# Performance work log

Measured on AMD Instinct MI355X. Metric: run time of the kernel, lower is better.

Reference implementation:

```python
import jax, jax.numpy as jnp
import numpy as np

EPS = 1e-5   # BatchNorm3d eps
SLOPE = 0.01 # LeakyReLU default negative_slope

def conv3(x, w, pad):
    return jax.lax.conv_general_dilated(
        x, w, (1, 1, 1), [(pad, pad)] * 3,
        dimension_numbers=('NCDHW', 'OIDHW', 'NCDHW'))

def bn(x):
    # BatchNorm3d in training mode with affine init (weight=1, bias=0):
    # normalize by per-channel batch statistics (biased variance).
    m = x.mean(axis=(0, 2, 3, 4), keepdims=True)
    v = x.var(axis=(0, 2, 3, 4), keepdims=True)
    return (x - m) / jnp.sqrt(v + EPS)

def lrelu(x):
    return jnp.where(x >= 0, x, SLOPE * x)

def block(x, w1, w2):
    # ConvBlock: conv3x3x3 -> BN -> LeakyReLU, twice
    x = lrelu(bn(conv3(x, w1, 1)))
    return lrelu(bn(conv3(x, w2, 1)))

def maxpool2(x):
    # MaxPool3dMPS(kernel=2, stride=2, pad=0) == standard 2x2x2 maxpool
    B, C, D, H, W = x.shape
    return x.reshape(B, C, D // 2, 2, H // 2, 2, W // 2, 2).max(axis=(3, 5, 7))

def upconv_fft(x, w):
    # ConvTranspose3dMPS: nearest-neighbor upsample by stride=2 via repeat,
    # then per-(out,in)-channel CIRCULAR convolution implemented with FFTs
    # (weight zero-padded to the upsampled spatial shape). Vectorized here
    # over all channel pairs with a frequency-domain einsum; rfft is used
    # since all signals are real (identical math, half the memory).
    s = 2
    B, C, D, H, W = x.shape
    up = jnp.broadcast_to(x[:, :, :, None, :, None, :, None],
                          (B, C, D, s, H, s, W, s)).reshape(B, C, D * s, H * s, W * s)
    sp = up.shape[2:]
    X = jnp.fft.rfftn(up, axes=(2, 3, 4))                 # [B, Cin, D', H', Wf]
    Wf = jnp.fft.rfftn(w, s=sp, axes=(2, 3, 4))           # [Cout, Cin, D', H', Wf]
    Y = jnp.einsum('bidhw,oidhw->bodhw', X, Wf)
    return jnp.fft.irfftn(Y, s=sp, axes=(2, 3, 4))

def unet_fwd(x, wf1, wf2, wd1a, wd1b, wd2a, wd2b, wd3a, wd3b,
             wt1, wu1a, wu1b, wt2, wu2a, wu2b, wt3, wu3a, wu3b,
             w_final, b_final):
    x1 = block(x, wf1, wf2)                       # [B,16,64,64,64]
    x2 = block(maxpool2(x1), wd1a, wd1b)          # [B,32,32,32,32]
    x3 = block(maxpool2(x2), wd2a, wd2b)          # [B,64,16,16,16]
    x4 = block(maxpool2(x3), wd3a, wd3b)          # [B,128,8,8,8]

    def up(a, skip, wt, wa, wb):
        u = lrelu(bn(upconv_fft(a, wt)))
        return block(jnp.concatenate([skip, u], axis=1), wa, wb)

    a = up(x4, x3, wt1, wu1a, wu1b)               # [B,64,16,16,16]
    a = up(a, x2, wt2, wu2a, wu2b)                # [B,32,32,32,32]
    a = up(a, x1, wt3, wu3a, wu3b)                # [B,16,64,64,64]
    return conv3(a, w_final, 0) + b_final.reshape(1, -1, 1, 1, 1)

def setup_inputs() -> dict:
    key = jax.random.key(0)
    ks = jax.random.split(key, 32)
    def W(k, shape):
        fan = int(np.prod(shape[1:]))
        return jax.random.normal(k, shape, jnp.float32) * np.float32((2.0 / fan) ** 0.5)
    inp = {}
    inp['x'] = jax.random.normal(ks[0], (1, 1, 64, 64, 64), jnp.float32)
    shapes = {
        'wf1': (16, 1, 3, 3, 3),  'wf2': (16, 16, 3, 3, 3),
        'wd1a': (32, 16, 3, 3, 3), 'wd1b': (32, 32, 3, 3, 3),
        'wd2a': (64, 32, 3, 3, 3), 'wd2b': (64, 64, 3, 3, 3),
        'wd3a': (128, 64, 3, 3, 3), 'wd3b': (128, 128, 3, 3, 3),
        'wt1': (64, 128, 2, 2, 2), 'wu1a': (64, 128, 3, 3, 3), 'wu1b': (64, 64, 3, 3, 3),
        'wt2': (32, 64, 2, 2, 2),  'wu2a': (32, 64, 3, 3, 3),  'wu2b': (32, 32, 3, 3, 3),
        'wt3': (16, 32, 2, 2, 2),  'wu3a': (16, 32, 3, 3, 3),  'wu3b': (16, 16, 3, 3, 3),
        'w_final': (1, 16, 1, 1, 1),
    }
    for i, (name, sh) in enumerate(shapes.items()):
        inp[name] = W(ks[i + 1], sh)
    inp['b_final'] = jnp.zeros((1,), jnp.float32)
    return inp

def reference(x, wf1, wf2, wd1a, wd1b, wd2a, wd2b, wd3a, wd3b,
              wt1, wu1a, wu1b, wt2, wu2a, wu2b, wt3, wu3a, wu3b,
              w_final, b_final):
    return unet_fwd(x, wf1, wf2, wd1a, wd1b, wd2a, wd2b, wd3a, wd3b,
                    wt1, wu1a, wu1b, wt2, wu2a, wu2b, wt3, wu3a, wu3b,
                    w_final, b_final)
```

## Files before the change

### kernel.cpp

```cpp
#include <hip/hip_runtime.h>

#define EPS   1e-5f
#define SLOPE 0.01f

template <int CIN, int CC, int BT>
__global__ __launch_bounds__(BT) void conv3_q9(const float* __restrict__ in,
                                               const float* __restrict__ wt,
                                               float* __restrict__ part,
                                               int D, int H, int W) {
    const int V    = D * H * W;
    const int Cout = gridDim.x * 8;
    const int z    = blockIdx.z;
    const int cib  = z * CC;
    __shared__ float wlds[27 * CC * 8];
    const int co0 = blockIdx.x * 8;
    for (int i = threadIdx.x; i < 27 * CC * 8; i += BT) {
        const int co = i & 7;
        const int t2 = i >> 3;
        const int tap = t2 % 3;
        const int t3  = t2 / 3;
        const int ci  = t3 % CC;
        const int pl  = t3 / CC;
        wlds[i] = wt[((size_t)(co0 + co) * CIN + cib + ci) * 27 + pl * 3 + tap];
    }
    __syncthreads();

    const float* inz = in + (size_t)cib * V;
    const int v0 = (blockIdx.y * BT + threadIdx.x) * 4;
    const int w0 = v0 % W;
    const int h0 = (v0 / W) % H;
    const int d0 = v0 / (W * H);

    const bool mL = (w0 != 0);
    const bool mR = (w0 + 4 != W);
    const int  wl = w0 - (mL ? 1 : 0);
    const int  wr = w0 + (mR ? 4 : 3);

    float acc[32];
#pragma unroll
    for (int i = 0; i < 32; ++i) acc[i] = 0.f;

#pragma unroll 1
    for (int kd = 0; kd < 3; ++kd) {
#pragma unroll 1
        for (int kh = 0; kh < 3; ++kh) {
            const int zd = d0 + kd - 1, zh = h0 + kh - 1;
            const bool okp = ((unsigned)zd < (unsigned)D) & ((unsigned)zh < (unsigned)H);
            const int row = okp ? (zd * H + zh) * W : 0;
            const int pl  = kd * 3 + kh;
            const float* wpl = &wlds[pl * CC * 24];
#pragma unroll 2
            for (int ci = 0; ci < CC; ++ci) {
                const float* p = inz + (size_t)ci * V + row;
                float4 m = *(const float4*)(p + w0);
                float lv = p[wl];
                float rv = p[wr];
                if (!okp) { m.x = 0.f; m.y = 0.f; m.z = 0.f; m.w = 0.f; }
                if (!(okp && mL)) lv = 0.f;
                if (!(okp && mR)) rv = 0.f;
                const float* wb = wpl + ci * 24;
                const float4 w0a = *(const float4*)(wb);
                const float4 w0b = *(const float4*)(wb + 4);
                const float4 w1a = *(const float4*)(wb + 8);
                const float4 w1b = *(const float4*)(wb + 12);
                const float4 w2a = *(const float4*)(wb + 16);
                const float4 w2b = *(const float4*)(wb + 20);
#define FMA4(A0, A1, A2, AP)                                                    \
                {                                                               \
                    float* a = (AP);                                            \
                    a[0] = fmaf(lv,  (A0), fmaf(m.x, (A1), fmaf(m.y, (A2), a[0])));\
                    a[1] = fmaf(m.x, (A0), fmaf(m.y, (A1), fmaf(m.z, (A2), a[1])));\
                    a[2] = fmaf(m.y, (A0), fmaf(m.z, (A1), fmaf(m.w, (A2), a[2])));\
                    a[3] = fmaf(m.z, (A0), fmaf(m.w, (A1), fmaf(rv,  (A2), a[3])));\
                }
                FMA4(w0a.x, w0b.x, w1a.x, acc + 0);
#undef FMA4
                (void)0;
#define FMA4C(A0, A1, A2, AP)                                                   \
                {                                                               \
                    float* a = (AP);                                            \
                    a[0] = fmaf(lv,  (A0), fmaf(m.x, (A1), fmaf(m.y, (A2), a[0])));\
                    a[1] = fmaf(m.x, (A0), fmaf(m.y, (A1), fmaf(m.z, (A2), a[1])));\
                    a[2] = fmaf(m.y, (A0), fmaf(m.z, (A1), fmaf(m.w, (A2), a[2])));\
                    a[3] = fmaf(m.z, (A0), fmaf(m.w, (A1), fmaf(rv,  (A2), a[3])));\
                }
                FMA4C(w0a.y, w1a.y, w2a.y, acc + 4);
                FMA4C(w0a.z, w1a.z, w2a.z, acc + 8);
                FMA4C(w0a.w, w1a.w, w2a.w, acc + 12);
                FMA4C(w0b.x, w1b.x, w2b.x, acc + 16);
                FMA4C(w0b.y, w1b.y, w2b.y, acc + 20);
                FMA4C(w0b.z, w1b.z, w2b.z, acc + 24);
                FMA4C(w0b.w, w1b.w, w2b.w, acc + 28);
#undef FMA4C
            }
        }
    }
#pragma unroll
    for (int co = 0; co < 8; ++co)
        *(float4*)&part[((size_t)z * Cout + co0 + co) * V + v0] = *(const float4*)&acc[co * 4];
}

template <int CIN, int CC, int BT>
__global__ __launch_bounds__(BT) void conv3_qA(const float* __restrict__ in,
                                               const float* __restrict__ wt,
                                               float* __restrict__ part,
                                               int D, int H, int W) {
    const int V    = D * H * W;
    const int Cout = gridDim.x * 8;
    const int z    = blockIdx.z;
    const int cib  = z * CC;
    __shared__ float wlds[27 * CC * 8];
    const int co0 = blockIdx.x * 8;
    for (int i = threadIdx.x; i < 27 * CC * 8; i += BT) {
        const int co  = i & 7;
        const int t2  = i >> 3;
        const int tap = t2 % 3;
        const int t3  = t2 / 3;
        const int ci  = t3 % CC;
        const int pl  = t3 / CC;
        wlds[i] = wt[((size_t)(co0 + co) * CIN + cib + ci) * 27 + pl * 3 + tap];
    }
    __syncthreads();

    const float* inz = in + (size_t)cib * V;
    const int v0 = (blockIdx.y * BT + threadIdx.x) * 4;
    const int w0 = v0 % W;
    const int h0 = (v0 / W) % H;
    const int d0 = v0 / (W * H);

    const bool mL = (w0 != 0);
    const bool mR = (w0 + 4 != W);
    const int  wl = w0 - (mL ? 1 : 0);
    const int  wr = w0 + (mR ? 4 : 3);

    float acc[32];
#pragma unroll
    for (int i = 0; i < 32; ++i) acc[i] = 0.f;

#pragma unroll 1
    for (int kd = 0; kd < 3; ++kd) {
#pragma unroll 1
        for (int kh = 0; kh < 3; ++kh) {
            const int zd = d0 + kd - 1, zh = h0 + kh - 1;
            const bool okp = ((unsigned)zd < (unsigned)D) & ((unsigned)zh < (unsigned)H);
            const int row = okp ? (zd * H + zh) * W : 0;
            const float* wpl = &wlds[(kd * 3 + kh) * CC * 24];
#pragma unroll 2
            for (int ci = 0; ci < CC; ++ci) {
                const float* p = inz + (size_t)ci * V + row;
                float4 m = *(const float4*)(p + w0);
                float lv = p[wl];
                float rv = p[wr];
                if (!okp) { m.x = 0.f; m.y = 0.f; m.z = 0.f; m.w = 0.f; }
                if (!(okp && mL)) lv = 0.f;
                if (!(okp && mR)) rv = 0.f;
                const float* wb = wpl + ci * 24;
                const float4 t0a = *(const float4*)(wb);
                const float4 t0b = *(const float4*)(wb + 4);
                const float4 t1a = *(const float4*)(wb + 8);
                const float4 t1b = *(const float4*)(wb + 12);
                const float4 t2a = *(const float4*)(wb + 16);
                const float4 t2b = *(const float4*)(wb + 20);
#define FMA4C(A0, A1, A2, AP)                                                       \
                {                                                                   \
                    float* a = (AP);                                                \
                    a[0] = fmaf(lv,  (A0), fmaf(m.x, (A1), fmaf(m.y, (A2), a[0]))); \
                    a[1] = fmaf(m.x, (A0), fmaf(m.y, (A1), fmaf(m.z, (A2), a[1]))); \
                    a[2] = fmaf(m.y, (A0), fmaf(m.z, (A1), fmaf(m.w, (A2), a[2]))); \
                    a[3] = fmaf(m.z, (A0), fmaf(m.w, (A1), fmaf(rv,  (A2), a[3]))); \
                }
                FMA4C(t0a.x, t1a.x, t2a.x, acc + 0);
                FMA4C(t0a.y, t1a.y, t2a.y, acc + 4);
                FMA4C(t0a.z, t1a.z, t2a.z, acc + 8);
                FMA4C(t0a.w, t1a.w, t2a.w, acc + 12);
                FMA4C(t0b.x, t1b.x, t2b.x, acc + 16);
                FMA4C(t0b.y, t1b.y, t2b.y, acc + 20);
                FMA4C(t0b.z, t1b.z, t2b.z, acc + 24);
                FMA4C(t0b.w, t1b.w, t2b.w, acc + 28);
#undef FMA4C
            }
        }
    }
#pragma unroll
    for (int co = 0; co < 8; ++co)
        *(float4*)&part[((size_t)z * Cout + co0 + co) * V + v0] = *(const float4*)&acc[co * 4];
}

template <int CIN, int CC, int VOXB>
__global__ __launch_bounds__(256) void upconv_v8(const float* __restrict__ in,
                                                 const float* __restrict__ wt,
                                                 float* __restrict__ part,
                                                 int Di, int Hi, int Wi) {
    const int Do = 2 * Di, Ho = 2 * Hi, Wo = 2 * Wi;
    const int Vo = Do * Ho * Wo;
    const int Vi = Di * Hi * Wi;
    const int Cout = gridDim.x * 8;
    const int z    = blockIdx.z;
    const int cib  = z * CC;
    __shared__ float wlds[8 * CC * 8];
    const int co0 = blockIdx.x * 8;
    for (int i = threadIdx.x; i < 8 * CC * 8; i += 256) {
        const int co  = i & 7;
        const int t2  = i >> 3;
        const int ci  = t2 % CC;
        const int tap = t2 / CC;
        wlds[i] = wt[((size_t)(co0 + co) * CIN + cib + ci) * 8 + tap];
    }
    __syncthreads();

    const float* inz = in + (size_t)cib * Vi;
    const int vbase = blockIdx.y * (256 * VOXB) + threadIdx.x;
    int od[VOXB], oh[VOXB], ow[VOXB];
#pragma unroll
    for (int j = 0; j < VOXB; ++j) {
        const int v = vbase + j * 256;
        ow[j] = v % Wo;
        oh[j] = (v / Wo) % Ho;
        od[j] = v / (Wo * Ho);
    }
    float acc[8 * VOXB];
#pragma unroll
    for (int i = 0; i < 8 * VOXB; ++i) acc[i] = 0.f;

#pragma unroll 1
    for (int kd = 0; kd < 2; ++kd)
#pragma unroll 1
    for (int kh = 0; kh < 2; ++kh)
#pragma unroll
    for (int kw = 0; kw < 2; ++kw) {
        const int tap = (kd * 2 + kh) * 2 + kw;
        int sp[VOXB];
#pragma unroll
        for (int j = 0; j < VOXB; ++j) {
            const int id = ((od[j] - kd + Do) & (Do - 1)) >> 1;
            const int ih = ((oh[j] - kh + Ho) & (Ho - 1)) >> 1;
            const int iw = ((ow[j] - kw + Wo) & (Wo - 1)) >> 1;
            sp[j] = (id * Hi + ih) * Wi + iw;
        }
        const float* wrow = &wlds[tap * CC * 8];
#pragma unroll 2
        for (int ci = 0; ci < CC; ++ci) {
            float xv[VOXB];
#pragma unroll
            for (int j = 0; j < VOXB; ++j)
                xv[j] = inz[(size_t)ci * Vi + sp[j]];
            const float4 wa = *(const float4*)(wrow + ci * 8);
            const float4 wb = *(const float4*)(wrow + ci * 8 + 4);
#define UF(WC, CO)                                                              \
            {                                                                   \
                _Pragma("unroll")                                               \
                for (int j = 0; j < VOXB; ++j)                                  \
                    acc[(CO) * VOXB + j] = fmaf(xv[j], (WC), acc[(CO) * VOXB + j]); \
            }
            UF(wa.x, 0) UF(wa.y, 1) UF(wa.z, 2) UF(wa.w, 3)
            UF(wb.x, 4) UF(wb.y, 5) UF(wb.z, 6) UF(wb.w, 7)
#undef UF
        }
    }
#pragma unroll
    for (int co = 0; co < 8; ++co)
#pragma unroll
        for (int j = 0; j < VOXB; ++j)
            part[((size_t)z * Cout + co0 + co) * Vo + vbase + j * 256] = acc[co * VOXB + j];
}

__global__ __launch_bounds__(256) void bn_stats_part_v2(const float* __restrict__ part,
                                                        float* __restrict__ pstat,
                                                        int C, int V, int S, int chunk) {
    const int c = blockIdx.x, seg = blockIdx.y;
    const size_t base = (size_t)c * V + (size_t)seg * chunk;
    float s1 = 0.f, s2 = 0.f;
    for (int i = threadIdx.x * 4; i < chunk; i += 1024) {
        float4 t = make_float4(0.f, 0.f, 0.f, 0.f);
        for (int s = 0; s < S; ++s) {
            const float4 v = *(const float4*)(part + (size_t)s * C * V + base + i);
            t.x += v.x; t.y += v.y; t.z += v.z; t.w += v.w;
        }
        s1 += t.x + t.y + t.z + t.w;
        s2 = fmaf(t.x, t.x, fmaf(t.y, t.y, fmaf(t.z, t.z, fmaf(t.w, t.w, s2))));
    }
#pragma unroll
    for (int off = 32; off > 0; off >>= 1) {
        s1 += __shfl_down(s1, off, 64);
        s2 += __shfl_down(s2, off, 64);
    }
    __shared__ float sh[8];
    const int wid  = threadIdx.x >> 6;
    const int lane = threadIdx.x & 63;
    if (lane == 0) { sh[wid] = s1; sh[4 + wid] = s2; }
    __syncthreads();
    if (threadIdx.x == 0) {
        pstat[(c * gridDim.y + seg) * 2]     = sh[0] + sh[1] + sh[2] + sh[3];
        pstat[(c * gridDim.y + seg) * 2 + 1] = sh[4] + sh[5] + sh[6] + sh[7];
    }
}

__global__ __launch_bounds__(64) void bn_stats_final(const float* __restrict__ pstat,
                                                     float* __restrict__ stats,
                                                     int S, int V) {
    const int c = blockIdx.x;
    float s1 = 0.f, s2 = 0.f;
    if ((int)threadIdx.x < S) {
        s1 = pstat[(c * S + threadIdx.x) * 2];
        s2 = pstat[(c * S + threadIdx.x) * 2 + 1];
    }
#pragma unroll
    for (int off = 32; off > 0; off >>= 1) {
        s1 += __shfl_down(s1, off, 64);
        s2 += __shfl_down(s2, off, 64);
    }
    if (threadIdx.x == 0) {
        const float inv  = 1.f / (float)V;
        const float mean = s1 * inv;
        const float var  = s2 * inv - mean * mean;
        stats[2 * c]     = mean;
        stats[2 * c + 1] = rsqrtf(var + EPS);
    }
}

__global__ __launch_bounds__(256) void bn_apply_v3(const float* __restrict__ part,
                                                   float* __restrict__ dst,
                                                   const float* __restrict__ stats,
                                                   int C, int V4, int S, int total4) {
    const int idx = blockIdx.x * blockDim.x + threadIdx.x;
    if (idx >= total4) return;
    const int c = idx / V4;
    const int v = idx - c * V4;
    const float4* p4 = (const float4*)part;
    float4 t = make_float4(0.f, 0.f, 0.f, 0.f);
    for (int s = 0; s < S; ++s) {
        const float4 x = p4[(size_t)(s * C + c) * V4 + v];
        t.x += x.x; t.y += x.y; t.z += x.z; t.w += x.w;
    }
    const float mean = stats[2 * c];
    const float rstd = stats[2 * c + 1];
    float u;
    u = (t.x - mean) * rstd; t.x = u >= 0.f ? u : SLOPE * u;
    u = (t.y - mean) * rstd; t.y = u >= 0.f ? u : SLOPE * u;
    u = (t.z - mean) * rstd; t.z = u >= 0.f ? u : SLOPE * u;
    u = (t.w - mean) * rstd; t.w = u >= 0.f ? u : SLOPE * u;
    ((float4*)dst)[idx] = t;
}

__global__ __launch_bounds__(256) void maxpool_kernel(const float* __restrict__ in,
                                                      float* __restrict__ out,
                                                      int D, int H, int W, int total) {
    const int Do = D >> 1, Ho = H >> 1, Wo = W >> 1;
    const int Vo = Do * Ho * Wo;
    const int idx = blockIdx.x * blockDim.x + threadIdx.x;
    if (idx >= total) return;
    const int c  = idx / Vo;
    const int v  = idx - c * Vo;
    const int ow = v % Wo;
    const int oh = (v / Wo) % Ho;
    const int od = v / (Wo * Ho);
    const size_t HW = (size_t)H * W;
    const float* p = in + (size_t)c * D * HW + (size_t)(2 * od) * HW + (size_t)(2 * oh) * W + 2 * ow;
    float m = p[0];
    m = fmaxf(m, p[1]);
    m = fmaxf(m, p[W]);
    m = fmaxf(m, p[W + 1]);
    m = fmaxf(m, p[HW]);
    m = fmaxf(m, p[HW + 1]);
    m = fmaxf(m, p[HW + W]);
    m = fmaxf(m, p[HW + W + 1]);
    out[idx] = m;
}

__global__ __launch_bounds__(256) void final_v2(const float* __restrict__ in,
                                                const float* __restrict__ w,
                                                const float* __restrict__ b,
                                                float* __restrict__ out, int C, int V4) {
    const int idx = blockIdx.x * blockDim.x + threadIdx.x;
    if (idx >= V4) return;
    const float bb = b[0];
    float4 acc = make_float4(bb, bb, bb, bb);
    for (int c = 0; c < C; ++c) {
        const float4 v = ((const float4*)in)[(size_t)c * V4 + idx];
        const float wc = w[c];
        acc.x = fmaf(v.x, wc, acc.x);
        acc.y = fmaf(v.y, wc, acc.y);
        acc.z = fmaf(v.z, wc, acc.z);
        acc.w = fmaf(v.w, wc, acc.w);
    }
    ((float4*)out)[idx] = acc;
}


extern "C" void kernel_launch(void* const* d_in, const int* in_sizes, int n_in,
                              void* d_out, int out_size, void* d_ws, size_t ws_size,
                              hipStream_t stream) {
    const float* x      = (const float*)d_in[0];
    const float* wf1    = (const float*)d_in[1];
    const float* wf2    = (const float*)d_in[2];
    const float* wd1a   = (const float*)d_in[3];
    const float* wd1b   = (const float*)d_in[4];
    const float* wd2a   = (const float*)d_in[5];
    const float* wd2b   = (const float*)d_in[6];
    const float* wd3a   = (const float*)d_in[7];
    const float* wd3b   = (const float*)d_in[8];
    const float* wt1    = (const float*)d_in[9];
    const float* wu1a   = (const float*)d_in[10];
    const float* wu1b   = (const float*)d_in[11];
    const float* wt2    = (const float*)d_in[12];
    const float* wu2a   = (const float*)d_in[13];
    const float* wu2b   = (const float*)d_in[14];
    const float* wt3    = (const float*)d_in[15];
    const float* wu3a   = (const float*)d_in[16];
    const float* wu3b   = (const float*)d_in[17];
    const float* w_fin  = (const float*)d_in[18];
    const float* b_fin  = (const float*)d_in[19];
    float* out = (float*)d_out;

    const int V0 = 64 * 64 * 64;
    const int V1 = 32 * 32 * 32;
    const int V2 = 16 * 16 * 16;
    const int V3 = 8 * 8 * 8;

    float* ws    = (float*)d_ws;
    float* cat3  = ws;
    float* cat2  = cat3 + (size_t)32 * V0;
    float* cat1  = cat2 + (size_t)64 * V1;
    float* x4    = cat1 + (size_t)128 * V2;
    float* tA    = x4   + (size_t)128 * V3;
    float* tB    = tA   + (size_t)16 * V0;
    float* part  = tB   + (size_t)16 * V0;
    float* stats = part + (size_t)16 * V0;
    float* pstat = stats + 256;

    auto blocks = [](int n) { return (n + 255) / 256; };

    auto bn_lrelu = [&](const float* p, float* dstp, int C, int V, int S) {
        const int NSEG = (V >= V0) ? 16 : (V == V1) ? 8 : (V == V2) ? 2 : 1;
        hipLaunchKernelGGL(bn_stats_part_v2, dim3(C, NSEG), dim3(256), 0, stream,
                           p, pstat, C, V, S, V / NSEG);
        hipLaunchKernelGGL(bn_stats_final, dim3(C), dim3(64), 0, stream, pstat, stats, NSEG, V);
        const int total4 = C * V / 4;
        hipLaunchKernelGGL(bn_apply_v3, dim3(blocks(total4)), dim3(256), 0, stream,
                           p, dstp, stats, C, V / 4, S, total4);
    };
    auto maxpool = [&](const float* in, float* o, int C, int D, int H, int W) {
        const int total = C * (D / 2) * (H / 2) * (W / 2);
        hipLaunchKernelGGL(maxpool_kernel, dim3(blocks(total)), dim3(256), 0, stream,
                           in, o, D, H, W, total);
    };

#define CONVQ(CIN, CC, BT, in_, wt_, prt_, dst_, Cout, D_, H_, W_)                          \
    {                                                                                       \
        const int V_ = (D_) * (H_) * (W_);                                                  \
        const int S  = (CIN) / (CC);                                                        \
        dim3 g((Cout) / 8, V_ / (4 * (BT)), S);                                             \
        hipLaunchKernelGGL((conv3_qA<CIN, CC, BT>), g, dim3(BT), 0, stream,                 \
                           in_, wt_, prt_, D_, H_, W_);                                     \
        bn_lrelu(prt_, dst_, Cout, V_, S);                                                  \
    }
#define UPCONV(CIN, CC, VOXB, in_, wt_, prt_, dst_, Cout, Di_, Hi_, Wi_)                    \
    {                                                                                       \
        const int Vo_ = 8 * (Di_) * (Hi_) * (Wi_);                                          \
        const int S  = (CIN) / (CC);                                                        \
        dim3 g((Cout) / 8, Vo_ / (256 * (VOXB)), S);                                        \
        hipLaunchKernelGGL((upconv_v8<CIN, CC, VOXB>), g, dim3(256), 0, stream,             \
                           in_, wt_, prt_, Di_, Hi_, Wi_);                                  \
        bn_lrelu(prt_, dst_, Cout, Vo_, S);                                                 \
    }

    CONVQ(1,   1,  256, x,   wf1,  tA,   tA,          16, 64, 64, 64);
    CONVQ(16,  8,  256, tA,  wf2,  tB,   cat3,        16, 64, 64, 64);
    maxpool(cat3, tA, 16, 64, 64, 64);
    CONVQ(16,  8,  64,  tA,  wd1a, part, tB,          32, 32, 32, 32);
    CONVQ(32,  8,  64,  tB,  wd1b, part, cat2,        32, 32, 32, 32);
    maxpool(cat2, tA, 32, 32, 32, 32);
    CONVQ(32,  8,  64,  tA,  wd2a, part, tB,          64, 16, 16, 16);
    CONVQ(64,  8,  64,  tB,  wd2b, part, cat1,        64, 16, 16, 16);
    maxpool(cat1, tA, 64, 16, 16, 16);
    CONVQ(64,  4,  64,  tA,  wd3a, part, tB,         128, 8, 8, 8);
    CONVQ(128, 8,  64,  tB,  wd3b, part, x4,         128, 8, 8, 8);

    UPCONV(128, 16, 1, x4, wt1, part, cat1 + (size_t)64 * V2, 64, 8, 8, 8);
    CONVQ(128, 8,  64, cat1, wu1a, part, tA,          64, 16, 16, 16);
    CONVQ(64,  8,  64, tA,   wu1b, part, tB,          64, 16, 16, 16);

    UPCONV(64, 16, 1, tB, wt2, part, cat2 + (size_t)32 * V1, 32, 16, 16, 16);
    CONVQ(64, 16, 64, cat2, wu2a, part, tA,           32, 32, 32, 32);
    CONVQ(32, 8,  64, tA,   wu2b, part, tB,           32, 32, 32, 32);

    {
        float* up3dst = cat3 + (size_t)16 * V0;
        UPCONV(32, 32, 4, tB, wt3, up3dst, up3dst, 16, 32, 32, 32);
    }
    CONVQ(32, 16, 256, cat3, wu3a, tB,   tA,          16, 64, 64, 64);
    CONVQ(16, 8,  256, tA,   wu3b, cat3, tB,          16, 64, 64, 64);

    hipLaunchKernelGGL(final_v2, dim3(blocks(V0 / 4)), dim3(256), 0, stream,
                       tB, w_fin, b_fin, out, 16, V0 / 4);

#undef CONVQ
#undef UPCONV
}
```

Baseline: 1.054 ms.

## Fuse BN statistics into full-resolution conv and upconv kernels, drop split-K partials

For the 64^3 layers, the convolution now runs over all input channels in one block instead of splitting input channels across grid z, so no partial sums are written and re-reduced. Per-block sums and sums of squares are computed in the conv epilogue, and a new bn_apply_f kernel finishes the statistics and applies normalization plus LeakyReLU in a single pass. The last upconv gets a matching fused-stats kernel. This removes the separate stats passes over large activations, at the cost of less grid parallelism, larger LDS weight tiles (up to 27*32*8 floats), and variance computed as E[x^2]-mean^2 in fp32, which is less numerically stable.

```diff
diff --git a/kernel.cpp b/kernel.cpp
--- a/kernel.cpp
+++ b/kernel.cpp
@@ -3,34 +3,32 @@
 #define EPS   1e-5f
 #define SLOPE 0.01f
 
-template <int CIN, int CC, int BT>
-__global__ __launch_bounds__(BT) void conv3_q9(const float* __restrict__ in,
-                                               const float* __restrict__ wt,
-                                               float* __restrict__ part,
-                                               int D, int H, int W) {
-    const int V    = D * H * W;
-    const int Cout = gridDim.x * 8;
-    const int z    = blockIdx.z;
-    const int cib  = z * CC;
-    __shared__ float wlds[27 * CC * 8];
+template <int CIN, int BT>
+__global__ __launch_bounds__(BT) void conv3_big(const float* __restrict__ in,
+                                                const float* __restrict__ wt,
+                                                float* __restrict__ out,
+                                                float* __restrict__ bstat,
+                                                int D, int H, int W) {
+    const int V   = D * H * W;
+    const int NB  = gridDim.y;
     const int co0 = blockIdx.x * 8;
-    for (int i = threadIdx.x; i < 27 * CC * 8; i += BT) {
-        const int co = i & 7;
-        const int t2 = i >> 3;
-        const int tap = t2 % 3;
-        const int t3  = t2 / 3;
-        const int ci  = t3 % CC;
-        const int pl  = t3 / CC;
-        wlds[i] = wt[((size_t)(co0 + co) * CIN + cib + ci) * 27 + pl * 3 + tap];
-    }
-    __syncthreads();
-
-    const float* inz = in + (size_t)cib * V;
+    __shared__ float wlds[27 * CIN * 8];
+    __shared__ float sred[(BT / 64) * 16];
+    for (int i = threadIdx.x; i < 27 * CIN * 8; i += BT) {
+        const int co  = i & 7;
+        const int r   = i >> 3;
+        const int tap = r % 3;
+        const int r2  = r / 3;
+        const int pl  = r2 % 9;
+        const int ci  = r2 / 9;
+        wlds[i] = wt[((size_t)(co0 + co) * CIN + ci) * 27 + pl * 3 + tap];
+    }
+    __syncthreads();
+
     const int v0 = (blockIdx.y * BT + threadIdx.x) * 4;
     const int w0 = v0 % W;
     const int h0 = (v0 / W) % H;
     const int d0 = v0 / (W * H);
-
     const bool mL = (w0 != 0);
     const bool mR = (w0 + 4 != W);
     const int  wl = w0 - (mL ? 1 : 0);
@@ -41,63 +39,239 @@
     for (int i = 0; i < 32; ++i) acc[i] = 0.f;
 
 #pragma unroll 1
-    for (int kd = 0; kd < 3; ++kd) {
-#pragma unroll 1
-        for (int kh = 0; kh < 3; ++kh) {
-            const int zd = d0 + kd - 1, zh = h0 + kh - 1;
-            const bool okp = ((unsigned)zd < (unsigned)D) & ((unsigned)zh < (unsigned)H);
-            const int row = okp ? (zd * H + zh) * W : 0;
-            const int pl  = kd * 3 + kh;
-            const float* wpl = &wlds[pl * CC * 24];
-#pragma unroll 2
-            for (int ci = 0; ci < CC; ++ci) {
-                const float* p = inz + (size_t)ci * V + row;
+    for (int ci = 0; ci < CIN; ++ci) {
+        const float* pc = in + (size_t)ci * V;
+#pragma unroll 1
+        for (int kd = 0; kd < 3; ++kd) {
+#pragma unroll 1
+            for (int kh = 0; kh < 3; ++kh) {
+                const int zd = d0 + kd - 1, zh = h0 + kh - 1;
+                const bool okp = ((unsigned)zd < (unsigned)D) & ((unsigned)zh < (unsigned)H);
+                const int row = okp ? (zd * H + zh) * W : 0;
+                const float* p = pc + row;
                 float4 m = *(const float4*)(p + w0);
                 float lv = p[wl];
                 float rv = p[wr];
                 if (!okp) { m.x = 0.f; m.y = 0.f; m.z = 0.f; m.w = 0.f; }
                 if (!(okp && mL)) lv = 0.f;
                 if (!(okp && mR)) rv = 0.f;
-                const float* wb = wpl + ci * 24;
-                const float4 w0a = *(const float4*)(wb);
-                const float4 w0b = *(const float4*)(wb + 4);
-                const float4 w1a = *(const float4*)(wb + 8);
-                const float4 w1b = *(const float4*)(wb + 12);
-                const float4 w2a = *(const float4*)(wb + 16);
-                const float4 w2b = *(const float4*)(wb + 20);
-#define FMA4(A0, A1, A2, AP)                                                    \
-                {                                                               \
-                    float* a = (AP);                                            \
-                    a[0] = fmaf(lv,  (A0), fmaf(m.x, (A1), fmaf(m.y, (A2), a[0])));\
-                    a[1] = fmaf(m.x, (A0), fmaf(m.y, (A1), fmaf(m.z, (A2), a[1])));\
-                    a[2] = fmaf(m.y, (A0), fmaf(m.z, (A1), fmaf(m.w, (A2), a[2])));\
-                    a[3] = fmaf(m.z, (A0), fmaf(m.w, (A1), fmaf(rv,  (A2), a[3])));\
+                const float* wb = &wlds[((ci * 9 + kd * 3 + kh) * 3) * 8];
+                const float4 t0a = *(const float4*)(wb);
+                const float4 t0b = *(const float4*)(wb + 4);
+                const float4 t1a = *(const float4*)(wb + 8);
+                const float4 t1b = *(const float4*)(wb + 12);
+                const float4 t2a = *(const float4*)(wb + 16);
+                const float4 t2b = *(const float4*)(wb + 20);
+#define FMA4C(A0, A1, A2, AP)                                                       \
+                {                                                                   \
+                    float* a = (AP);                                                \
+                    a[0] = fmaf(lv,  (A0), fmaf(m.x, (A1), fmaf(m.y, (A2), a[0]))); \
+                    a[1] = fmaf(m.x, (A0), fmaf(m.y, (A1), fmaf(m.z, (A2), a[1]))); \
+                    a[2] = fmaf(m.y, (A0), fmaf(m.z, (A1), fmaf(m.w, (A2), a[2]))); \
+                    a[3] = fmaf(m.z, (A0), fmaf(m.w, (A1), fmaf(rv,  (A2), a[3]))); \
                 }
-                FMA4(w0a.x, w0b.x, w1a.x, acc + 0);
-#undef FMA4
-                (void)0;
-#define FMA4C(A0, A1, A2, AP)                                                   \
-                {                                                               \
-                    float* a = (AP);                                            \
-                    a[0] = fmaf(lv,  (A0), fmaf(m.x, (A1), fmaf(m.y, (A2), a[0])));\
-                    a[1] = fmaf(m.x, (A0), fmaf(m.y, (A1), fmaf(m.z, (A2), a[1])));\
-                    a[2] = fmaf(m.y, (A0), fmaf(m.z, (A1), fmaf(m.w, (A2), a[2])));\
-                    a[3] = fmaf(m.z, (A0), fmaf(m.w, (A1), fmaf(rv,  (A2), a[3])));\
-                }
-                FMA4C(w0a.y, w1a.y, w2a.y, acc + 4);
-                FMA4C(w0a.z, w1a.z, w2a.z, acc + 8);
-                FMA4C(w0a.w, w1a.w, w2a.w, acc + 12);
-                FMA4C(w0b.x, w1b.x, w2b.x, acc + 16);
-                FMA4C(w0b.y, w1b.y, w2b.y, acc + 20);
-                FMA4C(w0b.z, w1b.z, w2b.z, acc + 24);
-                FMA4C(w0b.w, w1b.w, w2b.w, acc + 28);
+                FMA4C(t0a.x, t1a.x, t2a.x, acc + 0);
+                FMA4C(t0a.y, t1a.y, t2a.y, acc + 4);
+                FMA4C(t0a.z, t1a.z, t2a.z, acc + 8);
+                FMA4C(t0a.w, t1a.w, t2a.w, acc + 12);
+                FMA4C(t0b.x, t1b.x, t2b.x, acc + 16);
+                FMA4C(t0b.y, t1b.y, t2b.y, acc + 20);
+                FMA4C(t0b.z, t1b.z, t2b.z, acc + 24);
+                FMA4C(t0b.w, t1b.w, t2b.w, acc + 28);
 #undef FMA4C
             }
         }
     }
 #pragma unroll
     for (int co = 0; co < 8; ++co)
-        *(float4*)&part[((size_t)z * Cout + co0 + co) * V + v0] = *(const float4*)&acc[co * 4];
+        *(float4*)&out[(size_t)(co0 + co) * V + v0] = *(const float4*)&acc[co * 4];
+
+    float s1[8], s2[8];
+#pragma unroll
+    for (int co = 0; co < 8; ++co) {
+        const float* a = &acc[co * 4];
+        s1[co] = a[0] + a[1] + a[2] + a[3];
+        s2[co] = fmaf(a[0], a[0], fmaf(a[1], a[1], fmaf(a[2], a[2], a[3] * a[3])));
+    }
+#pragma unroll
+    for (int off = 32; off > 0; off >>= 1)
+#pragma unroll
+        for (int co = 0; co < 8; ++co) {
+            s1[co] += __shfl_down(s1[co], off, 64);
+            s2[co] += __shfl_down(s2[co], off, 64);
+        }
+    const int lane = threadIdx.x & 63;
+    const int wv   = threadIdx.x >> 6;
+    if (lane == 0)
+#pragma unroll
+        for (int co = 0; co < 8; ++co) {
+            sred[(wv * 8 + co) * 2]     = s1[co];
+            sred[(wv * 8 + co) * 2 + 1] = s2[co];
+        }
+    __syncthreads();
+    if ((int)threadIdx.x < 8) {
+        float S1 = 0.f, S2 = 0.f;
+#pragma unroll
+        for (int w = 0; w < BT / 64; ++w) {
+            S1 += sred[(w * 8 + threadIdx.x) * 2];
+            S2 += sred[(w * 8 + threadIdx.x) * 2 + 1];
+        }
+        bstat[((size_t)(co0 + threadIdx.x) * NB + blockIdx.y) * 2]     = S1;
+        bstat[((size_t)(co0 + threadIdx.x) * NB + blockIdx.y) * 2 + 1] = S2;
+    }
+}
+
+template <int CIN>
+__global__ __launch_bounds__(256) void upconv_big(const float* __restrict__ in,
+                                                  const float* __restrict__ wt,
+                                                  float* __restrict__ out,
+                                                  float* __restrict__ bstat,
+                                                  int Di, int Hi, int Wi) {
+    const int Do = 2 * Di, Ho = 2 * Hi, Wo = 2 * Wi;
+    const int Vo = Do * Ho * Wo;
+    const int Vi = Di * Hi * Wi;
+    const int NB = gridDim.y;
+    const int co0 = blockIdx.x * 8;
+    __shared__ float wlds[8 * CIN * 8];
+    __shared__ float sred[4 * 16];
+    for (int i = threadIdx.x; i < 8 * CIN * 8; i += 256) {
+        const int co  = i & 7;
+        const int t2  = i >> 3;
+        const int ci  = t2 % CIN;
+        const int tap = t2 / CIN;
+        wlds[i] = wt[((size_t)(co0 + co) * CIN + ci) * 8 + tap];
+    }
+    __syncthreads();
+
+    const int vbase = blockIdx.y * 1024 + threadIdx.x;
+    int od[4], oh[4], ow[4];
+#pragma unroll
+    for (int j = 0; j < 4; ++j) {
+        const int v = vbase + j * 256;
+        ow[j] = v % Wo;
+        oh[j] = (v / Wo) % Ho;
+        od[j] = v / (Wo * Ho);
+    }
+    float acc[32];
+#pragma unroll
+    for (int i = 0; i < 32; ++i) acc[i] = 0.f;
+
+#pragma unroll 1
+    for (int kd = 0; kd < 2; ++kd)
+#pragma unroll 1
+    for (int kh = 0; kh < 2; ++kh)
+#pragma unroll
+    for (int kw = 0; kw < 2; ++kw) {
+        const int tap = (kd * 2 + kh) * 2 + kw;
+        int sp[4];
+#pragma unroll
+        for (int j = 0; j < 4; ++j) {
+            const int id = ((od[j] - kd + Do) & (Do - 1)) >> 1;
+            const int ih = ((oh[j] - kh + Ho) & (Ho - 1)) >> 1;
+            const int iw = ((ow[j] - kw + Wo) & (Wo - 1)) >> 1;
+            sp[j] = (id * Hi + ih) * Wi + iw;
+        }
+        const float* wrow = &wlds[tap * CIN * 8];
+#pragma unroll 2
+        for (int ci = 0; ci < CIN; ++ci) {
+            float xv[4];
+#pragma unroll
+            for (int j = 0; j < 4; ++j)
+                xv[j] = in[(size_t)ci * Vi + sp[j]];
+            const float4 wa = *(const float4*)(wrow + ci * 8);
+            const float4 wb = *(const float4*)(wrow + ci * 8 + 4);
+#define UF(WC, CO)                                                              \
+            {                                                                   \
+                _Pragma("unroll")                                               \
+                for (int j = 0; j < 4; ++j)                                     \
+                    acc[(CO) * 4 + j] = fmaf(xv[j], (WC), acc[(CO) * 4 + j]);   \
+            }
+            UF(wa.x, 0) UF(wa.y, 1) UF(wa.z, 2) UF(wa.w, 3)
+            UF(wb.x, 4) UF(wb.y, 5) UF(wb.z, 6) UF(wb.w, 7)
+#undef UF
+        }
+    }
+#pragma unroll
+    for (int co = 0; co < 8; ++co)
+#pragma unroll
+        for (int j = 0; j < 4; ++j)
+            out[(size_t)(co0 + co) * Vo + vbase + j * 256] = acc[co * 4 + j];
+
+    float s1[8], s2[8];
+#pragma unroll
+    for (int co = 0; co < 8; ++co) {
+        const float* a = &acc[co * 4];
+        s1[co] = a[0] + a[1] + a[2] + a[3];
+        s2[co] = fmaf(a[0], a[0], fmaf(a[1], a[1], fmaf(a[2], a[2], a[3] * a[3])));
+    }
+#pragma unroll
+    for (int off = 32; off > 0; off >>= 1)
+#pragma unroll
+        for (int co = 0; co < 8; ++co) {
+            s1[co] += __shfl_down(s1[co], off, 64);
+            s2[co] += __shfl_down(s2[co], off, 64);
+        }
+    const int lane = threadIdx.x & 63;
+    const int wv   = threadIdx.x >> 6;
+    if (lane == 0)
+#pragma unroll
+        for (int co = 0; co < 8; ++co) {
+            sred[(wv * 8 + co) * 2]     = s1[co];
+            sred[(wv * 8 + co) * 2 + 1] = s2[co];
+        }
+    __syncthreads();
+    if ((int)threadIdx.x < 8) {
+        float S1 = 0.f, S2 = 0.f;
+#pragma unroll
+        for (int w = 0; w < 4; ++w) {
+            S1 += sred[(w * 8 + threadIdx.x) * 2];
+            S2 += sred[(w * 8 + threadIdx.x) * 2 + 1];
+        }
+        bstat[((size_t)(co0 + threadIdx.x) * NB + blockIdx.y) * 2]     = S1;
+        bstat[((size_t)(co0 + threadIdx.x) * NB + blockIdx.y) * 2 + 1] = S2;
+    }
+}
+
+__global__ __launch_bounds__(256) void bn_apply_f(const float* __restrict__ prt,
+                                                  float* __restrict__ dst,
+                                                  const float* __restrict__ bstat,
+                                                  int NB, int V4, float invV) {
+    const int c = blockIdx.x;
+    float s1 = 0.f, s2 = 0.f;
+    for (int i = threadIdx.x; i < NB; i += 256) {
+        s1 += bstat[((size_t)c * NB + i) * 2];
+        s2 += bstat[((size_t)c * NB + i) * 2 + 1];
+    }
+#pragma unroll
+    for (int off = 32; off > 0; off >>= 1) {
+        s1 += __shfl_down(s1, off, 64);
+        s2 += __shfl_down(s2, off, 64);
+    }
+    __shared__ float sh[8];
+    __shared__ float mv[2];
+    const int lane = threadIdx.x & 63;
+    const int wv   = threadIdx.x >> 6;
+    if (lane == 0) { sh[wv] = s1; sh[4 + wv] = s2; }
+    __syncthreads();
+    if (threadIdx.x == 0) {
+        const float S1 = sh[0] + sh[1] + sh[2] + sh[3];
+        const float S2 = sh[4] + sh[5] + sh[6] + sh[7];
+        const float mean = S1 * invV;
+        const float var  = S2 * invV - mean * mean;
+        mv[0] = mean;
+        mv[1] = rsqrtf(var + EPS);
+    }
+    __syncthreads();
+    const float mean = mv[0];
+    const float rstd = mv[1];
+    const int pos = blockIdx.y * 256 + threadIdx.x;
+    float4 t = ((const float4*)prt)[(size_t)c * V4 + pos];
+    float u;
+    u = (t.x - mean) * rstd; t.x = u >= 0.f ? u : SLOPE * u;
+    u = (t.y - mean) * rstd; t.y = u >= 0.f ? u : SLOPE * u;
+    u = (t.z - mean) * rstd; t.z = u >= 0.f ? u : SLOPE * u;
+    u = (t.w - mean) * rstd; t.w = u >= 0.f ? u : SLOPE * u;
+    ((float4*)dst)[(size_t)c * V4 + pos] = t;
 }
 
 template <int CIN, int CC, int BT>
@@ -427,6 +601,7 @@
     float* part  = tB   + (size_t)16 * V0;
     float* stats = part + (size_t)16 * V0;
     float* pstat = stats + 256;
+    float* bstat = pstat + 4096;
 
     auto blocks = [](int n) { return (n + 255) / 256; };
 
@@ -445,6 +620,15 @@
                            in, o, D, H, W, total);
     };
 
+#define CONVBIG(CIN, in_, wt_, prt_, dst_, Cout)                                            \
+    {                                                                                       \
+        const int NBv = V0 / (4 * 128);                                                     \
+        dim3 g((Cout) / 8, NBv);                                                            \
+        hipLaunchKernelGGL((conv3_big<CIN, 128>), g, dim3(128), 0, stream,                  \
+                           in_, wt_, prt_, bstat, 64, 64, 64);                              \
+        hipLaunchKernelGGL(bn_apply_f, dim3(Cout, V0 / 4 / 256), dim3(256), 0, stream,      \
+                           prt_, dst_, bstat, NBv, V0 / 4, 1.f / V0);                       \
+    }
 #define CONVQ(CIN, CC, BT, in_, wt_, prt_, dst_, Cout, D_, H_, W_)                          \
     {                                                                                       \
         const int V_ = (D_) * (H_) * (W_);                                                  \
@@ -464,8 +648,8 @@
         bn_lrelu(prt_, dst_, Cout, Vo_, S);                                                 \
     }
 
-    CONVQ(1,   1,  256, x,   wf1,  tA,   tA,          16, 64, 64, 64);
-    CONVQ(16,  8,  256, tA,  wf2,  tB,   cat3,        16, 64, 64, 64);
+    CONVBIG(1,  x,  wf1, tA, tA,   16);
+    CONVBIG(16, tA, wf2, tB, cat3, 16);
     maxpool(cat3, tA, 16, 64, 64, 64);
     CONVQ(16,  8,  64,  tA,  wd1a, part, tB,          32, 32, 32, 32);
     CONVQ(32,  8,  64,  tB,  wd1b, part, cat2,        32, 32, 32, 32);
@@ -486,14 +670,20 @@
 
     {
         float* up3dst = cat3 + (size_t)16 * V0;
-        UPCONV(32, 32, 4, tB, wt3, up3dst, up3dst, 16, 32, 32, 32);
-    }
-    CONVQ(32, 16, 256, cat3, wu3a, tB,   tA,          16, 64, 64, 64);
-    CONVQ(16, 8,  256, tA,   wu3b, cat3, tB,          16, 64, 64, 64);
+        const int NBv = V0 / 1024;
+        dim3 g(2, NBv);
+        hipLaunchKernelGGL((upconv_big<32>), g, dim3(256), 0, stream,
+                           tB, wt3, up3dst, bstat, 32, 32, 32);
+        hipLaunchKernelGGL(bn_apply_f, dim3(16, V0 / 4 / 256), dim3(256), 0, stream,
+                           up3dst, up3dst, bstat, NBv, V0 / 4, 1.f / V0);
+    }
+    CONVBIG(32, cat3, wu3a, tB,   tA, 16);
+    CONVBIG(16, tA,   wu3b, cat3, tB, 16);
 
     hipLaunchKernelGGL(final_v2, dim3(blocks(V0 / 4)), dim3(256), 0, stream,
                        tB, w_fin, b_fin, out, 16, V0 / 4);
 
+#undef CONVBIG
 #undef CONVQ
 #undef UPCONV
 }
```

New measurement: 1.080 ms. 1.03x slower.
